# Performance work log

Hardware: AMD Instinct MI355X
Metric: run time of the kernel (lower is better)

The kernel has to match this reference:

```python
import jax, jax.numpy as jnp
import numpy as np

N_STATE = 1024
N_HEAD = 16
B = 2
S = 2048


def setup_inputs() -> dict:
    key = jax.random.key(0)
    ks = jax.random.split(key, 8)
    s = 0.02
    x = jax.random.normal(ks[0], (B, S, N_STATE), dtype=jnp.float32)
    # causal additive mask, as in Whisper: upper triangle = -inf
    mask = jnp.where(jnp.triu(jnp.ones((S, S), dtype=bool), k=1), -jnp.inf, 0.0).astype(jnp.float32)
    Wq = jax.random.normal(ks[1], (N_STATE, N_STATE), dtype=jnp.float32) * s
    bq = jax.random.normal(ks[2], (N_STATE,), dtype=jnp.float32) * s
    Wk = jax.random.normal(ks[3], (N_STATE, N_STATE), dtype=jnp.float32) * s
    Wv = jax.random.normal(ks[4], (N_STATE, N_STATE), dtype=jnp.float32) * s
    bv = jax.random.normal(ks[5], (N_STATE,), dtype=jnp.float32) * s
    Wo = jax.random.normal(ks[6], (N_STATE, N_STATE), dtype=jnp.float32) * s
    bo = jax.random.normal(ks[7], (N_STATE,), dtype=jnp.float32) * s
    return {"x": x, "mask": mask, "Wq": Wq, "bq": bq, "Wk": Wk,
            "Wv": Wv, "bv": bv, "Wo": Wo, "bo": bo}


def reference(x, mask, Wq, bq, Wk, Wv, bv, Wo, bo):
    Bb, S_, D = x.shape
    H = N_HEAD
    hd = D // H
    scale = hd ** (-0.25)  # scale split across q and k, as in the source
    q = x @ Wq.T + bq              # [B,S,D]
    k = x @ Wk.T                   # key has no bias
    v = x @ Wv.T + bv
    # [B,S,D] -> [B,H,S,hd]
    q = q.reshape(Bb, S_, H, hd).transpose(0, 2, 1, 3) * scale
    k = k.reshape(Bb, S_, H, hd).transpose(0, 2, 1, 3) * scale
    v = v.reshape(Bb, S_, H, hd).transpose(0, 2, 1, 3)
    qk = jnp.einsum('bhsd,bhtd->bhst', q, k) + mask[:S_, :S_]
    w = jax.nn.softmax(qk, axis=-1).astype(q.dtype)
    out = jnp.einsum('bhst,bhtd->bhsd', w, v)
    out = out.transpose(0, 2, 1, 3).reshape(Bb, S_, D)
    return out @ Wo.T + bo
```

## Files before the change

### kernel.cpp

```cpp
#include <hip/hip_runtime.h>
#include <hip/hip_bf16.h>
#include <cmath>

typedef __bf16 bf16;
typedef __bf16 bf16x8 __attribute__((ext_vector_type(8)));
typedef __bf16 bf16x4 __attribute__((ext_vector_type(4)));
typedef float f32x4 __attribute__((ext_vector_type(4)));

#define QS 0.18033688f

__device__ __forceinline__ void load16_to_lds(const void* g, void* l) {
    __builtin_amdgcn_global_load_lds(
        (const __attribute__((address_space(1))) unsigned int*)g,
        (__attribute__((address_space(3))) unsigned int*)l, 16, 0, 0);
}

__global__ __launch_bounds__(256) void convert_kernel(
    const float* __restrict__ x,  const float* __restrict__ wq,
    const float* __restrict__ wk, const float* __restrict__ wv,
    const float* __restrict__ wo, bf16* __restrict__ dst)
{
    const size_t M1 = 1024ull * 1024ull, M4 = 4ull * M1;
    size_t i0 = ((size_t)blockIdx.x * 256 + threadIdx.x) * 8;
    const float* s;
    size_t off;
    float sc = 1.f;
    if      (i0 < M4)        { s = x;  off = i0; }
    else if (i0 < M4 + M1)   { s = wq; off = i0 - M4; sc = QS; }
    else if (i0 < M4 + 2*M1) { s = wk; off = i0 - M4 - M1; }
    else if (i0 < M4 + 3*M1) { s = wv; off = i0 - M4 - 2*M1; }
    else                     { s = wo; off = i0 - M4 - 3*M1; }
    float4 a = *(const float4*)(s + off);
    float4 b = *(const float4*)(s + off + 4);
    bf16x8 r = { (bf16)(a.x*sc), (bf16)(a.y*sc), (bf16)(a.z*sc), (bf16)(a.w*sc),
                 (bf16)(b.x*sc), (bf16)(b.y*sc), (bf16)(b.z*sc), (bf16)(b.w*sc) };
    *(bf16x8*)(dst + i0) = r;
}

template<int BM, int MODE>
__device__ __forceinline__ void gemm_core(
    const bf16* __restrict__ A, const bf16* __restrict__ W,
    const float* __restrict__ bias, void* __restrict__ C,
    int mb, int nb, float bias_scale)
{
    constexpr int IF = BM / 32;
    __shared__ __align__(16) bf16 As[BM * 32];
    __shared__ __align__(16) bf16 Bs[128 * 32];

    const int tid  = threadIdx.x;
    const int lane = tid & 63;
    const int wave = tid >> 6;
    const int wr   = (wave >> 1) * (BM / 2);
    const int wc   = (wave & 1) * 64;
    const int l15  = lane & 15;
    const int l4   = lane >> 4;
    const int swz  = (l4 ^ ((l15 >> 1) & 3)) * 8;

    f32x4 acc[IF][4] = {};

    for (int kt = 0; kt < 32; ++kt) {
#pragma unroll
        for (int it = 0; it < BM / 64; ++it) {
            int c = it * 256 + tid;
            int scol = ((c & 3) ^ ((c >> 3) & 3)) * 8;
            load16_to_lds(&A[(size_t)(mb * BM + (c >> 2)) * 1024 + kt * 32 + scol],
                          &As[(it * 256 + (tid & 192)) * 8]);
        }
#pragma unroll
        for (int it = 0; it < 2; ++it) {
            int c = it * 256 + tid;
            int scol = ((c & 3) ^ ((c >> 3) & 3)) * 8;
            load16_to_lds(&W[(size_t)(nb * 128 + (c >> 2)) * 1024 + kt * 32 + scol],
                          &Bs[(it * 256 + (tid & 192)) * 8]);
        }
        __syncthreads();
        bf16x8 af[IF], bfr[4];
#pragma unroll
        for (int i = 0; i < IF; ++i)
            af[i] = *(const bf16x8*)&As[(wr + i * 16 + l15) * 32 + swz];
#pragma unroll
        for (int j = 0; j < 4; ++j)
            bfr[j] = *(const bf16x8*)&Bs[(wc + j * 16 + l15) * 32 + swz];
#pragma unroll
        for (int i = 0; i < IF; ++i)
#pragma unroll
            for (int j = 0; j < 4; ++j)
                acc[i][j] = __builtin_amdgcn_mfma_f32_16x16x32_bf16(
                    af[i], bfr[j], acc[i][j], 0, 0, 0);
        __syncthreads();
    }

    if (MODE == 1 || MODE == 2) {
#pragma unroll
        for (int j = 0; j < 4; ++j) {
            int D = nb * 128 + wc + j * 16 + l15;
            float bv = bias ? bias[D] : 0.f;
            int hh = D >> 6, d = D & 63;
#pragma unroll
            for (int i = 0; i < IF; ++i) {
                int S0 = mb * BM + wr + i * 16 + l4 * 4;
#pragma unroll
                for (int r = 0; r < 4; ++r) {
                    int S = S0 + r;
                    int bb = S >> 11, key = S & 2047;
                    int bh = bb * 16 + hh, nt = key >> 6, ktl = key & 63;
                    size_t idx;
                    if (MODE == 1)
                        idx = ((size_t)(bh * 32 + nt) * 8 + (d >> 5) * 4 + (ktl >> 4)) * 512
                            + ((d >> 3) & 3) * 128 + (ktl & 15) * 8 + (d & 7);
                    else
                        idx = ((size_t)(bh * 32 + nt) * 8 + (ktl >> 5) * 4 + (d >> 4)) * 512
                            + ((ktl >> 3) & 3) * 128 + (d & 15) * 8 + (ktl & 7);
                    ((bf16*)C)[idx] = (bf16)(acc[i][j][r] + bv);
                }
            }
        }
    } else {
#pragma unroll
        for (int j = 0; j < 4; ++j) {
            int col = nb * 128 + wc + j * 16 + l15;
            float bv = bias ? bias[col] * bias_scale : 0.f;
#pragma unroll
            for (int i = 0; i < IF; ++i) {
                int row0 = mb * BM + wr + i * 16 + l4 * 4;
#pragma unroll
                for (int r = 0; r < 4; ++r) {
                    float val = acc[i][j][r] + bv;
                    size_t idx = (size_t)(row0 + r) * 1024 + col;
                    if (MODE == 3) ((float*)C)[idx] = val;
                    else           ((bf16*)C)[idx]  = (bf16)val;
                }
            }
        }
    }
}

__global__ __launch_bounds__(256) void qkv_kernel(
    const bf16* __restrict__ xb,
    const bf16* __restrict__ wqb, const float* __restrict__ bq,
    const bf16* __restrict__ wkb,
    const bf16* __restrict__ wvb, const float* __restrict__ bv,
    bf16* __restrict__ q, bf16* __restrict__ kfb, bf16* __restrict__ vfb)
{
    int mb = blockIdx.x;
    int nbg = blockIdx.y;
    int sel = nbg >> 3, nb = nbg & 7;
    if      (sel == 0) gemm_core<128, 0>(xb, wqb, bq,      q,   mb, nb, QS);
    else if (sel == 1) gemm_core<128, 1>(xb, wkb, nullptr, kfb, mb, nb, 1.f);
    else               gemm_core<128, 2>(xb, wvb, bv,      vfb, mb, nb, 1.f);
}

__global__ __launch_bounds__(256) void oproj_kernel(
    const bf16* __restrict__ ao, const bf16* __restrict__ wob,
    const float* __restrict__ bo, float* __restrict__ out)
{
    gemm_core<128, 3>(ao, wob, bo, out, blockIdx.x, blockIdx.y, 1.f);
}

__global__ __launch_bounds__(64, 2) void attn_kernel(
    const bf16* __restrict__ q, const bf16* __restrict__ kfb,
    const bf16* __restrict__ vfb, bf16* __restrict__ o,
    float* __restrict__ pbuf)
{
    __shared__ __align__(16) bf16 Ps[64 * 72];

    const int lane = threadIdx.x;
    const int l15  = lane & 15;
    const int l4   = lane >> 4;

    const int bh    = blockIdx.x;
    const int yy    = blockIdx.y;
    const int wt    = 31 - (yy >> 2);
    const int chunk = yy & 3;
    const int b  = bh >> 4, h = bh & 15;
    const int qrow0 = wt * 64;

    const int n   = wt + 1;
    const int nch = (n + 7) >> 3;
    if (chunk >= nch) return;
    const int nt0 = chunk * 8;
    const int nt1 = (nt0 + 8 < n) ? (nt0 + 8) : n;

    bf16x8 qf[4][2];
#pragma unroll
    for (int qb = 0; qb < 4; ++qb)
#pragma unroll
        for (int kk = 0; kk < 2; ++kk)
            qf[qb][kk] = *(const bf16x8*)&q[(size_t)(b * 2048 + qrow0 + qb * 16 + l15) * 1024
                                           + h * 64 + kk * 32 + l4 * 8];

    const bf16* kb = kfb + (size_t)bh * 131072;
    const bf16* vb = vfb + (size_t)bh * 131072;

    f32x4 oacc[4][4] = {};
    float lsum[4] = { 0.f, 0.f, 0.f, 0.f };

    for (int nt = nt0; nt < nt1; ++nt) {
        const bf16* kt_ = kb + nt * 4096;
        const bf16* vt_ = vb + nt * 4096;

        bf16x8 kf[2][4], vf[2][4];
#pragma unroll
        for (int kk = 0; kk < 2; ++kk)
#pragma unroll
            for (int j = 0; j < 4; ++j) {
                kf[kk][j] = *(const bf16x8*)&kt_[(kk * 4 + j) * 512 + lane * 8];
                vf[kk][j] = *(const bf16x8*)&vt_[(kk * 4 + j) * 512 + lane * 8];
            }

        const bool diag = (nt == n - 1);
#pragma unroll
        for (int qb = 0; qb < 4; ++qb) {
            f32x4 s[4] = {};
#pragma unroll
            for (int kk = 0; kk < 2; ++kk)
#pragma unroll
                for (int j = 0; j < 4; ++j)
                    s[j] = __builtin_amdgcn_mfma_f32_16x16x32_bf16(
                        kf[kk][j], qf[qb][kk], s[j], 0, 0, 0);

            float pv[4][4];
            if (diag) {
                int qg = qrow0 + qb * 16 + l15;
#pragma unroll
                for (int j = 0; j < 4; ++j)
#pragma unroll
                    for (int r = 0; r < 4; ++r) {
                        int kg = nt * 64 + j * 16 + l4 * 4 + r;
                        pv[j][r] = (kg > qg) ? 0.f : __builtin_amdgcn_exp2f(s[j][r]);
                    }
            } else {
#pragma unroll
                for (int j = 0; j < 4; ++j)
#pragma unroll
                    for (int r = 0; r < 4; ++r)
                        pv[j][r] = __builtin_amdgcn_exp2f(s[j][r]);
            }
#pragma unroll
            for (int j = 0; j < 4; ++j)
                lsum[qb] += (pv[j][0] + pv[j][1]) + (pv[j][2] + pv[j][3]);

#pragma unroll
            for (int j = 0; j < 4; ++j) {
                bf16x4 pk = { (bf16)pv[j][0], (bf16)pv[j][1], (bf16)pv[j][2], (bf16)pv[j][3] };
                *(bf16x4*)&Ps[(qb * 16 + l15) * 72 + j * 16 + l4 * 4] = pk;
            }
        }

#pragma unroll
        for (int kk = 0; kk < 2; ++kk) {
            bf16x8 pf[4];
#pragma unroll
            for (int qb = 0; qb < 4; ++qb)
                pf[qb] = *(const bf16x8*)&Ps[(qb * 16 + l15) * 72 + kk * 32 + l4 * 8];
#pragma unroll
            for (int f = 0; f < 4; ++f)
#pragma unroll
                for (int qb = 0; qb < 4; ++qb)
                    oacc[qb][f] = __builtin_amdgcn_mfma_f32_16x16x32_bf16(
                        pf[qb], vf[kk][f], oacc[qb][f], 0, 0, 0);
        }
    }

    if (nch == 1) {
#pragma unroll
        for (int qb = 0; qb < 4; ++qb) {
            float ls = lsum[qb];
            ls += __shfl_xor(ls, 16, 64);
            ls += __shfl_xor(ls, 32, 64);
            float rinv[4];
#pragma unroll
            for (int r = 0; r < 4; ++r) rinv[r] = 1.f / __shfl(ls, l4 * 4 + r, 64);
#pragma unroll
            for (int f = 0; f < 4; ++f)
#pragma unroll
                for (int r = 0; r < 4; ++r)
                    o[(size_t)(b * 2048 + qrow0 + qb * 16 + l4 * 4 + r) * 1024 + h * 64 + f * 16 + l15]
                        = (bf16)(oacc[qb][f][r] * rinv[r]);
        }
    } else {
        float* ps = pbuf + ((size_t)(bh * 32 + wt) * 4 + chunk) * 4160;
#pragma unroll
        for (int qb = 0; qb < 4; ++qb) {
            float ls = lsum[qb];
            ls += __shfl_xor(ls, 16, 64);
            ls += __shfl_xor(ls, 32, 64);
            if (l4 == 0) ps[4096 + qb * 16 + l15] = ls;
#pragma unroll
            for (int f = 0; f < 4; ++f)
#pragma unroll
                for (int r = 0; r < 4; ++r)
                    ps[(qb * 16 + l4 * 4 + r) * 64 + f * 16 + l15] = oacc[qb][f][r];
        }
    }
}

__global__ __launch_bounds__(256) void combine_kernel(
    const float* __restrict__ pbuf, bf16* __restrict__ ao)
{
    const int bh = blockIdx.x;
    const int wt = 8 + blockIdx.y;
    const int b = bh >> 4, h = bh & 15;
    const int n   = wt + 1;
    const int nch = (n + 7) >> 3;

    const int tid = threadIdx.x;
    const int qq  = tid >> 2;
    const int d0  = (tid & 3) * 16;

    const float* base0 = pbuf + (size_t)(bh * 32 + wt) * 4 * 4160;

    float ls = 0.f;
    float acc[16] = {};
    for (int c = 0; c < nch; ++c) {
        const float* p = base0 + c * 4160;
        ls += p[4096 + qq];
#pragma unroll
        for (int g = 0; g < 4; ++g) {
            float4 a = *(const float4*)(p + qq * 64 + d0 + g * 4);
            acc[g*4+0] += a.x; acc[g*4+1] += a.y; acc[g*4+2] += a.z; acc[g*4+3] += a.w;
        }
    }
    float inv = 1.f / ls;
    bf16* dst = &ao[(size_t)(b * 2048 + wt * 64 + qq) * 1024 + h * 64 + d0];
    bf16x8 r0 = { (bf16)(acc[0]*inv), (bf16)(acc[1]*inv), (bf16)(acc[2]*inv), (bf16)(acc[3]*inv),
                  (bf16)(acc[4]*inv), (bf16)(acc[5]*inv), (bf16)(acc[6]*inv), (bf16)(acc[7]*inv) };
    bf16x8 r1 = { (bf16)(acc[8]*inv), (bf16)(acc[9]*inv), (bf16)(acc[10]*inv), (bf16)(acc[11]*inv),
                  (bf16)(acc[12]*inv), (bf16)(acc[13]*inv), (bf16)(acc[14]*inv), (bf16)(acc[15]*inv) };
    *(bf16x8*)dst = r0;
    *(bf16x8*)(dst + 8) = r1;
}

extern "C" void kernel_launch(void* const* d_in, const int* in_sizes, int n_in,
                              void* d_out, int out_size, void* d_ws, size_t ws_size,
                              hipStream_t stream)
{
    const float* x  = (const float*)d_in[0];
    const float* Wq = (const float*)d_in[2];
    const float* bq = (const float*)d_in[3];
    const float* Wk = (const float*)d_in[4];
    const float* Wv = (const float*)d_in[5];
    const float* bv = (const float*)d_in[6];
    const float* Wo = (const float*)d_in[7];
    const float* bo = (const float*)d_in[8];
    float* out = (float*)d_out;

    const size_t M1 = 1024ull * 1024ull, M4 = 4ull * M1;
    bf16* base = (bf16*)d_ws;
    bf16* xb  = base;
    bf16* wqb = base + M4;
    bf16* wkb = base + M4 + M1;
    bf16* wvb = base + M4 + 2 * M1;
    bf16* wob = base + M4 + 3 * M1;
    bf16* q   = base + 8 * M1;
    bf16* kfb = base + 12 * M1;
    bf16* vfb = base + 16 * M1;
    bf16* ao  = xb;
    float* pbuf = (float*)(base + 20 * M1);

    convert_kernel<<<4096, 256, 0, stream>>>(x, Wq, Wk, Wv, Wo, base);
    qkv_kernel<<<dim3(32, 24), 256, 0, stream>>>(xb, wqb, bq, wkb, wvb, bv, q, kfb, vfb);
    attn_kernel<<<dim3(32, 128), 64, 0, stream>>>(q, kfb, vfb, ao, pbuf);
    combine_kernel<<<dim3(32, 24), 256, 0, stream>>>(pbuf, ao);
    oproj_kernel<<<dim3(32, 8), 256, 0, stream>>>(ao, wob, bo, out);
}
```

Baseline: 190.3 us.

## Deepen GEMM K-tile to 64 and pack attention work items four waves per block

The GEMM core now stages 64-wide K tiles with an 8-way XOR swizzle and runs two MFMA sub-steps per tile. This halves the number of barrier-separated iterations at the cost of doubled LDS per block. The attention kernel changes from 64-thread blocks, many of which exit early, to 256-thread blocks whose four waves each take one (query tile, chunk) item from a compacted enumeration, so no empty blocks are launched. It also reuses one register array for K then V fragments to lower register pressure and fuses exp, row-sum and the P store.

After: 231.8 us. +21.8%, slower.

```diff
diff --git a/kernel.cpp b/kernel.cpp
--- a/kernel.cpp
+++ b/kernel.cpp
@@ -44,8 +44,8 @@
     int mb, int nb, float bias_scale)
 {
     constexpr int IF = BM / 32;
-    __shared__ __align__(16) bf16 As[BM * 32];
-    __shared__ __align__(16) bf16 Bs[128 * 32];
+    __shared__ __align__(16) bf16 As[BM * 64];
+    __shared__ __align__(16) bf16 Bs[128 * 64];
 
     const int tid  = threadIdx.x;
     const int lane = tid & 63;
@@ -54,39 +54,44 @@
     const int wc   = (wave & 1) * 64;
     const int l15  = lane & 15;
     const int l4   = lane >> 4;
-    const int swz  = (l4 ^ ((l15 >> 1) & 3)) * 8;
+    const int sw   = l15 & 7;
 
     f32x4 acc[IF][4] = {};
 
-    for (int kt = 0; kt < 32; ++kt) {
-#pragma unroll
-        for (int it = 0; it < BM / 64; ++it) {
+    for (int kt = 0; kt < 16; ++kt) {
+#pragma unroll
+        for (int it = 0; it < BM / 32; ++it) {
             int c = it * 256 + tid;
-            int scol = ((c & 3) ^ ((c >> 3) & 3)) * 8;
-            load16_to_lds(&A[(size_t)(mb * BM + (c >> 2)) * 1024 + kt * 32 + scol],
+            int scol = ((c & 7) ^ ((c >> 3) & 7)) * 8;
+            load16_to_lds(&A[(size_t)(mb * BM + (c >> 3)) * 1024 + kt * 64 + scol],
                           &As[(it * 256 + (tid & 192)) * 8]);
         }
 #pragma unroll
-        for (int it = 0; it < 2; ++it) {
+        for (int it = 0; it < 4; ++it) {
             int c = it * 256 + tid;
-            int scol = ((c & 3) ^ ((c >> 3) & 3)) * 8;
-            load16_to_lds(&W[(size_t)(nb * 128 + (c >> 2)) * 1024 + kt * 32 + scol],
+            int scol = ((c & 7) ^ ((c >> 3) & 7)) * 8;
+            load16_to_lds(&W[(size_t)(nb * 128 + (c >> 3)) * 1024 + kt * 64 + scol],
                           &Bs[(it * 256 + (tid & 192)) * 8]);
         }
         __syncthreads();
-        bf16x8 af[IF], bfr[4];
-#pragma unroll
-        for (int i = 0; i < IF; ++i)
-            af[i] = *(const bf16x8*)&As[(wr + i * 16 + l15) * 32 + swz];
-#pragma unroll
-        for (int j = 0; j < 4; ++j)
-            bfr[j] = *(const bf16x8*)&Bs[(wc + j * 16 + l15) * 32 + swz];
-#pragma unroll
-        for (int i = 0; i < IF; ++i)
+#pragma unroll
+        for (int kk = 0; kk < 2; ++kk) {
+            bf16x8 af[IF], bfr[4];
+#pragma unroll
+            for (int i = 0; i < IF; ++i)
+                af[i] = *(const bf16x8*)&As[(wr + i * 16 + l15) * 64
+                            + (((kk * 4 + l4) ^ sw) * 8)];
 #pragma unroll
             for (int j = 0; j < 4; ++j)
-                acc[i][j] = __builtin_amdgcn_mfma_f32_16x16x32_bf16(
-                    af[i], bfr[j], acc[i][j], 0, 0, 0);
+                bfr[j] = *(const bf16x8*)&Bs[(wc + j * 16 + l15) * 64
+                            + (((kk * 4 + l4) ^ sw) * 8)];
+#pragma unroll
+            for (int i = 0; i < IF; ++i)
+#pragma unroll
+                for (int j = 0; j < 4; ++j)
+                    acc[i][j] = __builtin_amdgcn_mfma_f32_16x16x32_bf16(
+                        af[i], bfr[j], acc[i][j], 0, 0, 0);
+        }
         __syncthreads();
     }
 
@@ -157,27 +162,32 @@
     gemm_core<128, 3>(ao, wob, bo, out, blockIdx.x, blockIdx.y, 1.f);
 }
 
-__global__ __launch_bounds__(64, 2) void attn_kernel(
+__global__ __launch_bounds__(256, 3) void attn_kernel(
     const bf16* __restrict__ q, const bf16* __restrict__ kfb,
     const bf16* __restrict__ vfb, bf16* __restrict__ o,
     float* __restrict__ pbuf)
 {
-    __shared__ __align__(16) bf16 Ps[64 * 72];
-
-    const int lane = threadIdx.x;
+    __shared__ __align__(16) bf16 Ps[4][64 * 72];
+
+    const int tid  = threadIdx.x;
+    const int lane = tid & 63;
+    const int wave = tid >> 6;
     const int l15  = lane & 15;
     const int l4   = lane >> 4;
 
-    const int bh    = blockIdx.x;
-    const int yy    = blockIdx.y;
-    const int wt    = 31 - (yy >> 2);
-    const int chunk = yy & 3;
+    const int bh = blockIdx.x;
     const int b  = bh >> 4, h = bh & 15;
+
+    const int i = blockIdx.y * 4 + wave;
+    int wt, chunk;
+    if (i < 32)      { wt = 31 - (i >> 2);          chunk = i & 3; }
+    else if (i < 56) { int j = i - 32; wt = 23 - j / 3;   chunk = j % 3; }
+    else if (i < 72) { int j = i - 56; wt = 15 - (j >> 1); chunk = j & 1; }
+    else             { wt = 7 - (i - 72);           chunk = 0; }
+
     const int qrow0 = wt * 64;
-
     const int n   = wt + 1;
-    const int nch = (n + 7) >> 3;
-    if (chunk >= nch) return;
+    const int nch = (wt + 8) >> 3;
     const int nt0 = chunk * 8;
     const int nt1 = (nt0 + 8 < n) ? (nt0 + 8) : n;
 
@@ -199,14 +209,12 @@
         const bf16* kt_ = kb + nt * 4096;
         const bf16* vt_ = vb + nt * 4096;
 
-        bf16x8 kf[2][4], vf[2][4];
+        bf16x8 fr[2][4];
 #pragma unroll
         for (int kk = 0; kk < 2; ++kk)
 #pragma unroll
-            for (int j = 0; j < 4; ++j) {
-                kf[kk][j] = *(const bf16x8*)&kt_[(kk * 4 + j) * 512 + lane * 8];
-                vf[kk][j] = *(const bf16x8*)&vt_[(kk * 4 + j) * 512 + lane * 8];
-            }
+            for (int j = 0; j < 4; ++j)
+                fr[kk][j] = *(const bf16x8*)&kt_[(kk * 4 + j) * 512 + lane * 8];
 
         const bool diag = (nt == n - 1);
 #pragma unroll
@@ -217,48 +225,53 @@
 #pragma unroll
                 for (int j = 0; j < 4; ++j)
                     s[j] = __builtin_amdgcn_mfma_f32_16x16x32_bf16(
-                        kf[kk][j], qf[qb][kk], s[j], 0, 0, 0);
-
-            float pv[4][4];
+                        fr[kk][j], qf[qb][kk], s[j], 0, 0, 0);
+
             if (diag) {
                 int qg = qrow0 + qb * 16 + l15;
 #pragma unroll
-                for (int j = 0; j < 4; ++j)
-#pragma unroll
-                    for (int r = 0; r < 4; ++r) {
-                        int kg = nt * 64 + j * 16 + l4 * 4 + r;
-                        pv[j][r] = (kg > qg) ? 0.f : __builtin_amdgcn_exp2f(s[j][r]);
-                    }
+                for (int j = 0; j < 4; ++j) {
+                    int kg0 = nt * 64 + j * 16 + l4 * 4;
+                    float e0 = (kg0 + 0 > qg) ? 0.f : __builtin_amdgcn_exp2f(s[j][0]);
+                    float e1 = (kg0 + 1 > qg) ? 0.f : __builtin_amdgcn_exp2f(s[j][1]);
+                    float e2 = (kg0 + 2 > qg) ? 0.f : __builtin_amdgcn_exp2f(s[j][2]);
+                    float e3 = (kg0 + 3 > qg) ? 0.f : __builtin_amdgcn_exp2f(s[j][3]);
+                    lsum[qb] += (e0 + e1) + (e2 + e3);
+                    bf16x4 pk = { (bf16)e0, (bf16)e1, (bf16)e2, (bf16)e3 };
+                    *(bf16x4*)&Ps[wave][(qb * 16 + l15) * 72 + j * 16 + l4 * 4] = pk;
+                }
             } else {
 #pragma unroll
-                for (int j = 0; j < 4; ++j)
-#pragma unroll
-                    for (int r = 0; r < 4; ++r)
-                        pv[j][r] = __builtin_amdgcn_exp2f(s[j][r]);
+                for (int j = 0; j < 4; ++j) {
+                    float e0 = __builtin_amdgcn_exp2f(s[j][0]);
+                    float e1 = __builtin_amdgcn_exp2f(s[j][1]);
+                    float e2 = __builtin_amdgcn_exp2f(s[j][2]);
+                    float e3 = __builtin_amdgcn_exp2f(s[j][3]);
+                    lsum[qb] += (e0 + e1) + (e2 + e3);
+                    bf16x4 pk = { (bf16)e0, (bf16)e1, (bf16)e2, (bf16)e3 };
+                    *(bf16x4*)&Ps[wave][(qb * 16 + l15) * 72 + j * 16 + l4 * 4] = pk;
+                }
             }
+        }
+
+#pragma unroll
+        for (int kk = 0; kk < 2; ++kk)
 #pragma unroll
             for (int j = 0; j < 4; ++j)
-                lsum[qb] += (pv[j][0] + pv[j][1]) + (pv[j][2] + pv[j][3]);
-
-#pragma unroll
-            for (int j = 0; j < 4; ++j) {
-                bf16x4 pk = { (bf16)pv[j][0], (bf16)pv[j][1], (bf16)pv[j][2], (bf16)pv[j][3] };
-                *(bf16x4*)&Ps[(qb * 16 + l15) * 72 + j * 16 + l4 * 4] = pk;
-            }
-        }
+                fr[kk][j] = *(const bf16x8*)&vt_[(kk * 4 + j) * 512 + lane * 8];
 
 #pragma unroll
         for (int kk = 0; kk < 2; ++kk) {
             bf16x8 pf[4];
 #pragma unroll
             for (int qb = 0; qb < 4; ++qb)
-                pf[qb] = *(const bf16x8*)&Ps[(qb * 16 + l15) * 72 + kk * 32 + l4 * 8];
+                pf[qb] = *(const bf16x8*)&Ps[wave][(qb * 16 + l15) * 72 + kk * 32 + l4 * 8];
 #pragma unroll
             for (int f = 0; f < 4; ++f)
 #pragma unroll
                 for (int qb = 0; qb < 4; ++qb)
                     oacc[qb][f] = __builtin_amdgcn_mfma_f32_16x16x32_bf16(
-                        pf[qb], vf[kk][f], oacc[qb][f], 0, 0, 0);
+                        pf[qb], fr[kk][f], oacc[qb][f], 0, 0, 0);
         }
     }
 
@@ -360,7 +373,7 @@
 
     convert_kernel<<<4096, 256, 0, stream>>>(x, Wq, Wk, Wv, Wo, base);
     qkv_kernel<<<dim3(32, 24), 256, 0, stream>>>(xb, wqb, bq, wkb, wvb, bv, q, kfb, vfb);
-    attn_kernel<<<dim3(32, 128), 64, 0, stream>>>(q, kfb, vfb, ao, pbuf);
+    attn_kernel<<<dim3(32, 20), 256, 0, stream>>>(q, kfb, vfb, ao, pbuf);
     combine_kernel<<<dim3(32, 24), 256, 0, stream>>>(pbuf, ao);
     oproj_kernel<<<dim3(32, 8), 256, 0, stream>>>(ao, wob, bo, out);
 }
```
